# Performance work log

Measured on AMD Instinct MI355X. Metric: run time of the kernel, lower is better.

## Reference

```python
import jax, jax.numpy as jnp
import numpy as np

EPS = 1e-6

def _rms_norm(t, g):
    # t: [B, S, C] (applied before the view to heads, matching the torch code)
    y = t.astype(jnp.float32)
    y = jax.lax.rsqrt(jnp.mean(y * y, axis=-1, keepdims=True) + EPS)
    return (t * y * g).astype(t.dtype)

def _apply_rope(t, cos, sin):
    # t: [B, S, N, D]; cos/sin: [1, S, 1, D//2]; interleaved pair rotation
    b, s, n, d = t.shape
    tr = t.reshape(b, s, n, d // 2, 2)
    tre, tim = tr[..., 0], tr[..., 1]
    out = jnp.stack([tre * cos - tim * sin, tre * sin + tim * cos], axis=-1)
    return out.reshape(b, s, n, d)

def setup_inputs() -> dict:
    key = jax.random.key(0)
    ks = jax.random.split(key, 8)
    B, S, DIM, N, D = 2, 1024, 3072, 24, 128
    x = jax.random.normal(ks[0], (B, S, DIM), dtype=jnp.float32)
    seq_lens = jax.random.randint(ks[1], (B,), S // 2, S + 1, dtype=jnp.int32)
    grid_sizes = jnp.tile(jnp.array([[16, 8, 8]], dtype=jnp.int32), (B, 1))
    # rope angle table [1024, D//2]: pos * inv_freq
    inv_freq = 1.0 / (10000.0 ** (jnp.arange(D // 2, dtype=jnp.float32) * 2.0 / D))
    freqs = jnp.arange(1024, dtype=jnp.float32)[:, None] * inv_freq[None, :]
    sc = 1.0 / np.sqrt(DIM)
    Wq = jax.random.normal(ks[2], (DIM, DIM), dtype=jnp.float32) * sc
    Wk = jax.random.normal(ks[3], (DIM, DIM), dtype=jnp.float32) * sc
    Wv = jax.random.normal(ks[4], (DIM, DIM), dtype=jnp.float32) * sc
    Wo = jax.random.normal(ks[5], (DIM, DIM), dtype=jnp.float32) * sc
    bq = jnp.zeros((DIM,), jnp.float32); bk = jnp.zeros((DIM,), jnp.float32)
    bv = jnp.zeros((DIM,), jnp.float32); bo = jnp.zeros((DIM,), jnp.float32)
    gq = jnp.ones((DIM,), jnp.float32); gk = jnp.ones((DIM,), jnp.float32)
    return {"x": x, "seq_lens": seq_lens, "grid_sizes": grid_sizes, "freqs": freqs,
            "Wq": Wq, "bq": bq, "Wk": Wk, "bk": bk, "Wv": Wv, "bv": bv,
            "Wo": Wo, "bo": bo, "gq": gq, "gk": gk}

def reference(x, seq_lens, grid_sizes, freqs, Wq, bq, Wk, bk, Wv, bv, Wo, bo, gq, gk):
    b, s, dim = x.shape
    d = 2 * freqs.shape[1]          # head_dim
    n = dim // d                    # num_heads
    q = _rms_norm(x @ Wq.T + bq, gq).reshape(b, s, n, d)
    k = _rms_norm(x @ Wk.T + bk, gk).reshape(b, s, n, d)
    v = (x @ Wv.T + bv).reshape(b, s, n, d)
    ang = freqs[:s]                 # [S, D//2]
    cos = jnp.cos(ang)[None, :, None, :]
    sin = jnp.sin(ang)[None, :, None, :]
    q = _apply_rope(q, cos, sin)
    k = _apply_rope(k, cos, sin)
    # full attention (window_size = (-1,-1)), varlen key masking via seq_lens
    scale = d ** -0.5
    scores = jnp.einsum('bind,bjnd->bnij', q, k) * scale   # [B,N,S,S]
    key_valid = jnp.arange(s)[None, :] < seq_lens[:, None]  # [B,S]
    scores = jnp.where(key_valid[:, None, None, :], scores, jnp.finfo(scores.dtype).min)
    p = jax.nn.softmax(scores, axis=-1)
    out = jnp.einsum('bnij,bjnd->bind', p, v).reshape(b, s, dim)
    return out @ Wo.T + bo
```

## Files before the change

kernel.cpp:

```cpp
#include <hip/hip_runtime.h>
#include <cmath>

#define BB   2
#define SS   1024
#define DIMM 3072
#define NHH  24
#define HDD  128
#define MM   (BB * SS)

typedef _Float16 f16;
typedef __attribute__((ext_vector_type(8))) _Float16 half8;
typedef __attribute__((ext_vector_type(4))) float floatx4;
typedef unsigned int u32;
typedef const __attribute__((address_space(1))) u32* gp1;
typedef __attribute__((address_space(3))) u32* lp3;

__device__ __forceinline__ void gload_lds16(const void* g, void* l) {
    __builtin_amdgcn_global_load_lds((gp1)g, (lp3)l, 16, 0, 0);
}

__global__ __launch_bounds__(256) void cvt_f16_kernel(
    const float* __restrict__ in, f16* __restrict__ outp, int n8)
{
    int i = blockIdx.x * 256 + threadIdx.x;
    if (i >= n8) return;
    const float4* p = (const float4*)(in + (size_t)i * 8);
    float4 a = p[0], b = p[1];
    half8 h = {(f16)a.x, (f16)a.y, (f16)a.z, (f16)a.w,
               (f16)b.x, (f16)b.y, (f16)b.z, (f16)b.w};
    *(half8*)(outp + (size_t)i * 8) = h;
}

template<bool QKV>
__global__ __launch_bounds__(256) void gemm_f16p(
    const f16* __restrict__ A,
    const f16* __restrict__ W0, const f16* __restrict__ W1, const f16* __restrict__ W2,
    const float* __restrict__ b0, const float* __restrict__ b1, const float* __restrict__ b2,
    f16* __restrict__ D0, f16* __restrict__ D1, f16* __restrict__ D2,
    float* __restrict__ F)
{
    constexpr int K = DIMM;
    constexpr int NSTEP = K / 64;
    __shared__ __align__(16) f16 As[128 * 64];
    __shared__ __align__(16) f16 Bs[128 * 64];

    const int tid  = threadIdx.x;
    const int lane = tid & 63;
    const int wave = tid >> 6;
    const int wm = wave >> 1, wn = wave & 1;
    const int lr = lane & 15;
    const int lq = lane >> 4;

    const int id  = blockIdx.x;
    const int cpx = (int)gridDim.x >> 3;
    const int swz = (id & 7) * cpx + (id >> 3);
    const int bm = (swz & 15) << 7;
    const int bn = (swz >> 4) << 7;

    const f16* Wh; const float* bias; f16* D = nullptr;
    int nloc = bn;
    if constexpr (QKV) {
        int sel = bn / DIMM;
        nloc = bn - sel * DIMM;
        Wh   = sel == 0 ? W0 : (sel == 1 ? W1 : W2);
        bias = sel == 0 ? b0 : (sel == 1 ? b1 : b2);
        D    = sel == 0 ? D0 : (sel == 1 ? D1 : D2);
    } else { Wh = W0; bias = b0; }

    const int srow = lane >> 3;
    const int scol = ((lane & 7) ^ srow) << 3;
    const f16* ag = A  + (size_t)(bm   + srow) * K + scol;
    const f16* bg = Wh + (size_t)(nloc + srow) * K + scol;

    floatx4 acc[4][4];
#pragma unroll
    for (int i = 0; i < 4; ++i)
#pragma unroll
        for (int j = 0; j < 4; ++j) acc[i][j] = (floatx4){0.f, 0.f, 0.f, 0.f};

    for (int ks = 0; ks < NSTEP; ++ks) {
        const int k0 = ks * 64;
        __syncthreads();
#pragma unroll
        for (int i = 0; i < 4; ++i) {
            int rbase = wave * 32 + i * 8;
            gload_lds16(ag + (size_t)rbase * K + k0, &As[rbase * 64]);
            gload_lds16(bg + (size_t)rbase * K + k0, &Bs[rbase * 64]);
        }
        __syncthreads();

#pragma unroll
        for (int sub = 0; sub < 2; ++sub) {
            half8 af[4], bf[4];
#pragma unroll
            for (int i = 0; i < 4; ++i) {
                int ra = wm * 64 + i * 16 + lr;
                int rb = wn * 64 + i * 16 + lr;
                af[i] = *(const half8*)&As[ra * 64 + ((((sub << 2) + lq) ^ (lr & 7)) << 3)];
                bf[i] = *(const half8*)&Bs[rb * 64 + ((((sub << 2) + lq) ^ (lr & 7)) << 3)];
            }
#pragma unroll
            for (int mi = 0; mi < 4; ++mi)
#pragma unroll
                for (int ni = 0; ni < 4; ++ni)
                    acc[mi][ni] = __builtin_amdgcn_mfma_f32_16x16x32_f16(af[mi], bf[ni], acc[mi][ni], 0, 0, 0);
        }
    }

    const int crow0 = bm + wm * 64 + (lq << 2);
    const int ccol0 = nloc + wn * 64;
#pragma unroll
    for (int ni = 0; ni < 4; ++ni) {
        const int col = ccol0 + ni * 16 + lr;
        const float bv = bias[col];
#pragma unroll
        for (int mi = 0; mi < 4; ++mi) {
            const int row = crow0 + mi * 16;
#pragma unroll
            for (int r2 = 0; r2 < 4; ++r2) {
                if constexpr (QKV)
                    D[(size_t)(row + r2) * DIMM + col] = (f16)(acc[mi][ni][r2] + bv);
                else
                    F[(size_t)(row + r2) * DIMM + col] = acc[mi][ni][r2] + bv;
            }
        }
    }
}

template<bool QKV>
__global__ __launch_bounds__(256) void gemm_f16m(
    const f16* __restrict__ A,
    const float* __restrict__ W0, const float* __restrict__ W1, const float* __restrict__ W2,
    const float* __restrict__ b0, const float* __restrict__ b1, const float* __restrict__ b2,
    f16* __restrict__ D0, f16* __restrict__ D1, f16* __restrict__ D2,
    float* __restrict__ F)
{
    constexpr int K = DIMM;
    constexpr int NSTEP = K / 32;
    __shared__ f16 As[128 * 32];
    __shared__ f16 Bs[128 * 32];

    const int tid  = threadIdx.x;
    const int lane = tid & 63;
    const int wave = tid >> 6;
    const int wm = wave >> 1, wn = wave & 1;
    const int lr = lane & 15;
    const int lq = lane >> 4;

    const int id  = blockIdx.x;
    const int cpx = (int)gridDim.x >> 3;
    const int swz = (id & 7) * cpx + (id >> 3);
    const int bm = (swz & 15) << 7;
    const int bn = (swz >> 4) << 7;

    const float* W; const float* bias; f16* D = nullptr;
    int nloc = bn;
    if constexpr (QKV) {
        int sel = bn / DIMM;
        nloc = bn - sel * DIMM;
        W    = sel == 0 ? W0 : (sel == 1 ? W1 : W2);
        bias = sel == 0 ? b0 : (sel == 1 ? b1 : b2);
        D    = sel == 0 ? D0 : (sel == 1 ? D1 : D2);
    } else { W = W0; bias = b0; }

    const int r0 = tid >> 2;
    const int c8 = (tid & 3) << 3;
    const float* bp0 = W + (size_t)(nloc + r0) * K + c8;
    const float* bp1 = W + (size_t)(nloc + r0 + 64) * K + c8;

    const int arow_l = lane >> 2;
    const int acol_l = (lane & 3) << 3;
    const f16* agbase = A + (size_t)bm * K;

    float4 sb00, sb01, sb10, sb11;
    auto LOADB = [&](int k0) {
        sb00 = *(const float4*)(bp0 + k0); sb01 = *(const float4*)(bp0 + k0 + 4);
        sb10 = *(const float4*)(bp1 + k0); sb11 = *(const float4*)(bp1 + k0 + 4);
    };
    auto STOREB = [&]() {
        half8 h0 = {(f16)sb00.x, (f16)sb00.y, (f16)sb00.z, (f16)sb00.w,
                    (f16)sb01.x, (f16)sb01.y, (f16)sb01.z, (f16)sb01.w};
        half8 h1 = {(f16)sb10.x, (f16)sb10.y, (f16)sb10.z, (f16)sb10.w,
                    (f16)sb11.x, (f16)sb11.y, (f16)sb11.z, (f16)sb11.w};
        *(half8*)&Bs[r0 * 32 + c8]        = h0;
        *(half8*)&Bs[(r0 + 64) * 32 + c8] = h1;
    };

    floatx4 acc[4][4];
#pragma unroll
    for (int i = 0; i < 4; ++i)
#pragma unroll
        for (int j = 0; j < 4; ++j) acc[i][j] = (floatx4){0.f, 0.f, 0.f, 0.f};

    LOADB(0);
    for (int ks = 0; ks < NSTEP; ++ks) {
        const int k0 = ks * 32;
        __syncthreads();
#pragma unroll
        for (int i = 0; i < 2; ++i) {
            int rbase = wave * 32 + i * 16;
            gload_lds16(agbase + (size_t)(rbase + arow_l) * K + k0 + acol_l,
                        &As[rbase * 32]);
        }
        STOREB();
        __syncthreads();
        if (ks + 1 < NSTEP) LOADB(k0 + 32);

        half8 af[4], bf[4];
#pragma unroll
        for (int i = 0; i < 4; ++i) {
            af[i] = *(const half8*)&As[(wm * 64 + i * 16 + lr) * 32 + lq * 8];
            bf[i] = *(const half8*)&Bs[(wn * 64 + i * 16 + lr) * 32 + lq * 8];
        }
#pragma unroll
        for (int mi = 0; mi < 4; ++mi)
#pragma unroll
            for (int ni = 0; ni < 4; ++ni)
                acc[mi][ni] = __builtin_amdgcn_mfma_f32_16x16x32_f16(af[mi], bf[ni], acc[mi][ni], 0, 0, 0);
    }

    const int crow0 = bm + wm * 64 + (lq << 2);
    const int ccol0 = nloc + wn * 64;
#pragma unroll
    for (int ni = 0; ni < 4; ++ni) {
        const int col = ccol0 + ni * 16 + lr;
        const float bv = bias[col];
#pragma unroll
        for (int mi = 0; mi < 4; ++mi) {
            const int row = crow0 + mi * 16;
#pragma unroll
            for (int r2 = 0; r2 < 4; ++r2) {
                if constexpr (QKV)
                    D[(size_t)(row + r2) * DIMM + col] = (f16)(acc[mi][ni][r2] + bv);
                else
                    F[(size_t)(row + r2) * DIMM + col] = acc[mi][ni][r2] + bv;
            }
        }
    }
}

__global__ __launch_bounds__(192) void rmsnorm_rope_f16(
    f16* __restrict__ q, f16* __restrict__ k,
    const float* __restrict__ gq, const float* __restrict__ gk,
    const float* __restrict__ freqs)
{
    f16* t = (blockIdx.y == 0) ? q : k;
    const float* g = (blockIdx.y == 0) ? gq : gk;
    const int row = blockIdx.x;
    const int s = row & (SS - 1);
    const int tid = threadIdx.x;
    f16* base = t + (size_t)row * DIMM + tid * 16;

    half8 v0 = *(const half8*)base;
    half8 v1 = *(const half8*)(base + 8);
    float v[16];
#pragma unroll
    for (int j = 0; j < 8; ++j) { v[j] = (float)v0[j]; v[8 + j] = (float)v1[j]; }

    float ssq = 0.f;
#pragma unroll
    for (int j = 0; j < 16; ++j) ssq += v[j] * v[j];
#pragma unroll
    for (int off = 32; off > 0; off >>= 1) ssq += __shfl_down(ssq, off, 64);
    __shared__ float red[3];
    if ((tid & 63) == 0) red[tid >> 6] = ssq;
    __syncthreads();
    float tot = red[0] + red[1] + red[2];
    float sc = rsqrtf(tot * (1.0f / (float)DIMM) + 1e-6f);

    const float* gp = g + tid * 16;
    float y[16];
#pragma unroll
    for (int j = 0; j < 16; ++j) y[j] = v[j] * sc * gp[j];

#pragma unroll
    for (int p = 0; p < 8; ++p) {
        int idx = tid * 16 + 2 * p;
        int f = (idx & 127) >> 1;
        float ang = freqs[s * 64 + f];
        float cc = cosf(ang), sn = sinf(ang);
        float e = y[2 * p], o = y[2 * p + 1];
        y[2 * p]     = e * cc - o * sn;
        y[2 * p + 1] = e * sn + o * cc;
    }
    half8 o0, o1;
#pragma unroll
    for (int j = 0; j < 8; ++j) { o0[j] = (f16)y[j]; o1[j] = (f16)y[8 + j]; }
    *(half8*)base       = o0;
    *(half8*)(base + 8) = o1;
}

__global__ __launch_bounds__(256) void flash_attn_f16(
    const f16* __restrict__ Q, const f16* __restrict__ K,
    const f16* __restrict__ V, const int* __restrict__ seq_lens,
    f16* __restrict__ O)
{
    __shared__ __align__(16) f16 QPs[64 * 128];
    __shared__ __align__(16) f16 Ks[64 * 128];
    __shared__ __align__(16) f16 Vt[128 * 64];

    const int tid  = threadIdx.x;
    const int lane = tid & 63;
    const int wave = tid >> 6;
    const int ln = lane & 15;
    const int lq = lane >> 4;
    const int i0 = blockIdx.x * 64;
    const int h  = blockIdx.y;
    const int b  = blockIdx.z;
    const int slen = seq_lens[b];
    const float scale = 0.08838834764831845f;
    const size_t gstride = NHH * HDD;

    const f16* Qg = Q + ((size_t)(b * SS + i0) * NHH + h) * HDD;
#pragma unroll
    for (int rep = 0; rep < 4; ++rep) {
        int u = tid + rep * 256;
        int r = u >> 4, d0 = (u & 15) << 3;
        half8 qv = *(const half8*)(Qg + (size_t)r * gstride + d0);
        *(half8*)(QPs + r * 128 + (d0 ^ ((r & 7) << 3))) = qv;
    }
    __syncthreads();

    half8 qfrag[4];
    {
        int rq = wave * 16 + ln;
#pragma unroll
        for (int ks = 0; ks < 4; ++ks)
            qfrag[ks] = *(const half8*)(QPs + rq * 128 + ((ks * 32 + lq * 8) ^ ((rq & 7) << 3)));
    }

    floatx4 accO[8];
#pragma unroll
    for (int dt = 0; dt < 8; ++dt) accO[dt] = (floatx4){0.f, 0.f, 0.f, 0.f};
    float mrow[4] = {-3.0e38f, -3.0e38f, -3.0e38f, -3.0e38f};
    float lrow[4] = {0.f, 0.f, 0.f, 0.f};

    const int nT = (slen + 63) >> 6;
    for (int t = 0; t < nT; ++t) {
        const int j0g = t * 64;
        __syncthreads();

        const f16* Kg = K + ((size_t)(b * SS + j0g) * NHH + h) * HDD;
#pragma unroll
        for (int rep = 0; rep < 4; ++rep) {
            int u = tid + rep * 256;
            int r = u >> 4, d0 = (u & 15) << 3;
            half8 kv = *(const half8*)(Kg + (size_t)r * gstride + d0);
            *(half8*)(Ks + r * 128 + (d0 ^ ((r & 7) << 3))) = kv;
        }
        const f16* Vg = V + ((size_t)(b * SS + j0g) * NHH + h) * HDD;
#pragma unroll
        for (int rep = 0; rep < 2; ++rep) {
            int u = tid + rep * 256;
            int jp = u & 31, j0 = jp * 2;
            int d0 = (u >> 5) << 3;
            half8 va = *(const half8*)(Vg + (size_t)j0 * gstride + d0);
            half8 vb = *(const half8*)(Vg + (size_t)(j0 + 1) * gstride + d0);
#pragma unroll
            for (int i = 0; i < 8; ++i) {
                int d = d0 + i;
                union { f16 h[2]; u32 w; } pk;
                pk.h[0] = va[i]; pk.h[1] = vb[i];
                *(u32*)(Vt + d * 64 + (j0 ^ ((d & 7) << 3))) = pk.w;
            }
        }
        __syncthreads();

        floatx4 acc_s[4];
#pragma unroll
        for (int nt = 0; nt < 4; ++nt) {
            acc_s[nt] = (floatx4){0.f, 0.f, 0.f, 0.f};
            int rk = nt * 16 + ln;
#pragma unroll
            for (int ks = 0; ks < 4; ++ks) {
                half8 kf = *(const half8*)(Ks + rk * 128 + ((ks * 32 + lq * 8) ^ ((rk & 7) << 3)));
                acc_s[nt] = __builtin_amdgcn_mfma_f32_16x16x32_f16(qfrag[ks], kf, acc_s[nt], 0, 0, 0);
            }
        }

        float s[4][4];
#pragma unroll
        for (int nt = 0; nt < 4; ++nt) {
            int j = j0g + nt * 16 + ln;
            bool valid = (j < slen);
#pragma unroll
            for (int r = 0; r < 4; ++r)
                s[nt][r] = valid ? acc_s[nt][r] * scale : -3.0e38f;
        }
        float fct[4];
#pragma unroll
        for (int r = 0; r < 4; ++r) {
            float m4 = fmaxf(fmaxf(s[0][r], s[1][r]), fmaxf(s[2][r], s[3][r]));
            m4 = fmaxf(m4, __shfl_xor(m4, 1, 64));
            m4 = fmaxf(m4, __shfl_xor(m4, 2, 64));
            m4 = fmaxf(m4, __shfl_xor(m4, 4, 64));
            m4 = fmaxf(m4, __shfl_xor(m4, 8, 64));
            float mn = fmaxf(mrow[r], m4);
            fct[r] = __expf(mrow[r] - mn);
            mrow[r] = mn;
            float ls = 0.f;
#pragma unroll
            for (int nt = 0; nt < 4; ++nt) {
                float p = __expf(s[nt][r] - mn);
                s[nt][r] = p;
                ls += p;
            }
            ls += __shfl_xor(ls, 1, 64);
            ls += __shfl_xor(ls, 2, 64);
            ls += __shfl_xor(ls, 4, 64);
            ls += __shfl_xor(ls, 8, 64);
            lrow[r] = lrow[r] * fct[r] + ls;
        }

#pragma unroll
        for (int nt = 0; nt < 4; ++nt) {
#pragma unroll
            for (int r = 0; r < 4; ++r) {
                int rw = lq * 4 + r;
                int j = nt * 16 + ln;
                QPs[(wave * 16 + rw) * 128 + (j ^ ((rw & 7) << 3))] = (f16)s[nt][r];
            }
        }

#pragma unroll
        for (int dt = 0; dt < 8; ++dt)
#pragma unroll
            for (int r = 0; r < 4; ++r) accO[dt][r] *= fct[r];

        half8 pfrag[2];
#pragma unroll
        for (int js = 0; js < 2; ++js)
            pfrag[js] = *(const half8*)(QPs + (wave * 16 + ln) * 128 + ((js * 32 + lq * 8) ^ ((ln & 7) << 3)));
#pragma unroll
        for (int dt = 0; dt < 8; ++dt) {
            int d = dt * 16 + ln;
#pragma unroll
            for (int js = 0; js < 2; ++js) {
                half8 vf = *(const half8*)(Vt + d * 64 + ((js * 32 + lq * 8) ^ ((d & 7) << 3)));
                accO[dt] = __builtin_amdgcn_mfma_f32_16x16x32_f16(pfrag[js], vf, accO[dt], 0, 0, 0);
            }
        }
    }

    float linv[4];
#pragma unroll
    for (int r = 0; r < 4; ++r) linv[r] = 1.0f / lrow[r];
    f16* Og = O + ((size_t)(b * SS + i0) * NHH + h) * HDD;
#pragma unroll
    for (int dt = 0; dt < 8; ++dt) {
#pragma unroll
        for (int r = 0; r < 4; ++r) {
            int qr = wave * 16 + lq * 4 + r;
            int d = dt * 16 + ln;
            Og[(size_t)qr * gstride + d] = (f16)(accO[dt][r] * linv[r]);
        }
    }
}

extern "C" void kernel_launch(void* const* d_in, const int* in_sizes, int n_in,
                              void* d_out, int out_size, void* d_ws, size_t ws_size,
                              hipStream_t stream)
{
    const float* x     = (const float*)d_in[0];
    const int*   seq   = (const int*)d_in[1];
    const float* freqs = (const float*)d_in[3];
    const float* Wq    = (const float*)d_in[4];
    const float* bq    = (const float*)d_in[5];
    const float* Wk    = (const float*)d_in[6];
    const float* bk    = (const float*)d_in[7];
    const float* Wv    = (const float*)d_in[8];
    const float* bv    = (const float*)d_in[9];
    const float* Wo    = (const float*)d_in[10];
    const float* bo    = (const float*)d_in[11];
    const float* gq    = (const float*)d_in[12];
    const float* gk    = (const float*)d_in[13];

    float* out = (float*)d_out;
    const size_t MD = (size_t)MM * DIMM;
    const size_t WD = (size_t)DIMM * DIMM;

    f16* X16 = (f16*)d_ws;
    f16* q16 = X16 + MD;
    f16* k16 = X16 + 2 * MD;
    f16* v16 = (f16*)d_out;

    const int nMD8 = (int)(MD / 8);
    const int nWD8 = (int)(WD / 8);
    const size_t need = (3 * MD + 3 * WD) * sizeof(f16);

    cvt_f16_kernel<<<nMD8 / 256, 256, 0, stream>>>(x, X16, nMD8);

    if (ws_size >= need) {
        f16* Wq16 = X16 + 3 * MD;
        f16* Wk16 = Wq16 + WD;
        f16* Wv16 = Wk16 + WD;
        f16* Wo16 = Wq16;
        cvt_f16_kernel<<<nWD8 / 256, 256, 0, stream>>>(Wq, Wq16, nWD8);
        cvt_f16_kernel<<<nWD8 / 256, 256, 0, stream>>>(Wk, Wk16, nWD8);
        cvt_f16_kernel<<<nWD8 / 256, 256, 0, stream>>>(Wv, Wv16, nWD8);
        gemm_f16p<true><<<(MM / 128) * (3 * DIMM / 128), 256, 0, stream>>>(
            X16, Wq16, Wk16, Wv16, bq, bk, bv, q16, k16, v16, nullptr);
        cvt_f16_kernel<<<nWD8 / 256, 256, 0, stream>>>(Wo, Wo16, nWD8);
        rmsnorm_rope_f16<<<dim3(MM, 2), 192, 0, stream>>>(q16, k16, gq, gk, freqs);
        flash_attn_f16<<<dim3(SS / 64, NHH, BB), 256, 0, stream>>>(q16, k16, v16, seq, X16);
        gemm_f16p<false><<<(MM / 128) * (DIMM / 128), 256, 0, stream>>>(
            X16, Wo16, nullptr, nullptr, bo, nullptr, nullptr, nullptr, nullptr, nullptr, out);
    } else {
        gemm_f16m<true><<<(MM / 128) * (3 * DIMM / 128), 256, 0, stream>>>(
            X16, Wq, Wk, Wv, bq, bk, bv, q16, k16, v16, nullptr);
        rmsnorm_rope_f16<<<dim3(MM, 2), 192, 0, stream>>>(q16, k16, gq, gk, freqs);
        flash_attn_f16<<<dim3(SS / 64, NHH, BB), 256, 0, stream>>>(q16, k16, v16, seq, X16);
        gemm_f16m<false><<<(MM / 128) * (DIMM / 128), 256, 0, stream>>>(
            X16, Wo, nullptr, nullptr, bo, nullptr, nullptr, nullptr, nullptr, nullptr, out);
    }
}
```

Before: 368.8 us.

## Double-buffer LDS tiles in f16 GEMM and merge QKV weight conversions

```diff
diff --git a/kernel.cpp b/kernel.cpp
--- a/kernel.cpp
+++ b/kernel.cpp
@@ -31,6 +31,21 @@
     *(half8*)(outp + (size_t)i * 8) = h;
 }
 
+__global__ __launch_bounds__(256) void cvt3_f16_kernel(
+    const float* __restrict__ w0, const float* __restrict__ w1,
+    const float* __restrict__ w2, f16* __restrict__ outp, int n8each)
+{
+    int i = blockIdx.x * 256 + threadIdx.x;
+    int sel = i / n8each;
+    int j = i - sel * n8each;
+    const float* in = sel == 0 ? w0 : (sel == 1 ? w1 : w2);
+    const float4* p = (const float4*)(in + (size_t)j * 8);
+    float4 a = p[0], b = p[1];
+    half8 h = {(f16)a.x, (f16)a.y, (f16)a.z, (f16)a.w,
+               (f16)b.x, (f16)b.y, (f16)b.z, (f16)b.w};
+    *(half8*)(outp + (size_t)i * 8) = h;
+}
+
 template<bool QKV>
 __global__ __launch_bounds__(256) void gemm_f16p(
     const f16* __restrict__ A,
@@ -41,8 +56,9 @@
 {
     constexpr int K = DIMM;
     constexpr int NSTEP = K / 64;
-    __shared__ __align__(16) f16 As[128 * 64];
-    __shared__ __align__(16) f16 Bs[128 * 64];
+    constexpr int TS = 128 * 64;
+    __shared__ __align__(16) f16 As[2][TS];
+    __shared__ __align__(16) f16 Bs[2][TS];
 
     const int tid  = threadIdx.x;
     const int lane = tid & 63;
@@ -72,22 +88,28 @@
     const f16* ag = A  + (size_t)(bm   + srow) * K + scol;
     const f16* bg = Wh + (size_t)(nloc + srow) * K + scol;
 
-    floatx4 acc[4][4];
-#pragma unroll
-    for (int i = 0; i < 4; ++i)
-#pragma unroll
-        for (int j = 0; j < 4; ++j) acc[i][j] = (floatx4){0.f, 0.f, 0.f, 0.f};
-
-    for (int ks = 0; ks < NSTEP; ++ks) {
-        const int k0 = ks * 64;
-        __syncthreads();
+    auto STAGE = [&](int t, int buf) {
+        const int k0 = t * 64;
 #pragma unroll
         for (int i = 0; i < 4; ++i) {
             int rbase = wave * 32 + i * 8;
-            gload_lds16(ag + (size_t)rbase * K + k0, &As[rbase * 64]);
-            gload_lds16(bg + (size_t)rbase * K + k0, &Bs[rbase * 64]);
-        }
-        __syncthreads();
+            gload_lds16(ag + (size_t)rbase * K + k0, &As[buf][rbase * 64]);
+            gload_lds16(bg + (size_t)rbase * K + k0, &Bs[buf][rbase * 64]);
+        }
+    };
+
+    floatx4 acc[4][4];
+#pragma unroll
+    for (int i = 0; i < 4; ++i)
+#pragma unroll
+        for (int j = 0; j < 4; ++j) acc[i][j] = (floatx4){0.f, 0.f, 0.f, 0.f};
+
+    STAGE(0, 0);
+    __syncthreads();
+
+    for (int ks = 0; ks < NSTEP; ++ks) {
+        const int cur = ks & 1;
+        if (ks + 1 < NSTEP) STAGE(ks + 1, cur ^ 1);
 
 #pragma unroll
         for (int sub = 0; sub < 2; ++sub) {
@@ -96,8 +118,8 @@
             for (int i = 0; i < 4; ++i) {
                 int ra = wm * 64 + i * 16 + lr;
                 int rb = wn * 64 + i * 16 + lr;
-                af[i] = *(const half8*)&As[ra * 64 + ((((sub << 2) + lq) ^ (lr & 7)) << 3)];
-                bf[i] = *(const half8*)&Bs[rb * 64 + ((((sub << 2) + lq) ^ (lr & 7)) << 3)];
+                af[i] = *(const half8*)&As[cur][ra * 64 + ((((sub << 2) + lq) ^ (lr & 7)) << 3)];
+                bf[i] = *(const half8*)&Bs[cur][rb * 64 + ((((sub << 2) + lq) ^ (lr & 7)) << 3)];
             }
 #pragma unroll
             for (int mi = 0; mi < 4; ++mi)
@@ -105,6 +127,7 @@
                 for (int ni = 0; ni < 4; ++ni)
                     acc[mi][ni] = __builtin_amdgcn_mfma_f32_16x16x32_f16(af[mi], bf[ni], acc[mi][ni], 0, 0, 0);
         }
+        __syncthreads();
     }
 
     const int crow0 = bm + wm * 64 + (lq << 2);
@@ -495,9 +518,7 @@
         f16* Wk16 = Wq16 + WD;
         f16* Wv16 = Wk16 + WD;
         f16* Wo16 = Wq16;
-        cvt_f16_kernel<<<nWD8 / 256, 256, 0, stream>>>(Wq, Wq16, nWD8);
-        cvt_f16_kernel<<<nWD8 / 256, 256, 0, stream>>>(Wk, Wk16, nWD8);
-        cvt_f16_kernel<<<nWD8 / 256, 256, 0, stream>>>(Wv, Wv16, nWD8);
+        cvt3_f16_kernel<<<3 * nWD8 / 256, 256, 0, stream>>>(Wq, Wk, Wv, Wq16, nWD8);
         gemm_f16p<true><<<(MM / 128) * (3 * DIMM / 128), 256, 0, stream>>>(
             X16, Wq16, Wk16, Wv16, bq, bk, bv, q16, k16, v16, nullptr);
         cvt_f16_kernel<<<nWD8 / 256, 256, 0, stream>>>(Wo, Wo16, nWD8);
```

New measurement: 371.9 us. Within noise of the previous version (+0.8%).

## Batch weight conversions into one launch and split Q projection into separate GEMM

Applied to the files above, without the earlier changes.

```diff
diff --git a/kernel.cpp b/kernel.cpp
--- a/kernel.cpp
+++ b/kernel.cpp
@@ -29,6 +29,114 @@
     half8 h = {(f16)a.x, (f16)a.y, (f16)a.z, (f16)a.w,
                (f16)b.x, (f16)b.y, (f16)b.z, (f16)b.w};
     *(half8*)(outp + (size_t)i * 8) = h;
+}
+
+__global__ __launch_bounds__(256) void cvt3_f16_kernel(
+    const float* __restrict__ w0, const float* __restrict__ w1,
+    const float* __restrict__ w2, f16* __restrict__ outp, int n8each)
+{
+    int i = blockIdx.x * 256 + threadIdx.x;
+    int sel = i / n8each;
+    int j = i - sel * n8each;
+    const float* in = sel == 0 ? w0 : (sel == 1 ? w1 : w2);
+    const float4* p = (const float4*)(in + (size_t)j * 8);
+    float4 a = p[0], b = p[1];
+    half8 h = {(f16)a.x, (f16)a.y, (f16)a.z, (f16)a.w,
+               (f16)b.x, (f16)b.y, (f16)b.z, (f16)b.w};
+    *(half8*)(outp + (size_t)i * 8) = h;
+}
+
+__global__ __launch_bounds__(256) void cvt4_f16_kernel(
+    const float* __restrict__ w0, const float* __restrict__ w1,
+    const float* __restrict__ w2, const float* __restrict__ w3,
+    f16* __restrict__ outp, int n8each)
+{
+    int i = blockIdx.x * 256 + threadIdx.x;
+    int sel = i / n8each;
+    int j = i - sel * n8each;
+    const float* in = sel == 0 ? w0 : (sel == 1 ? w1 : (sel == 2 ? w2 : w3));
+    const float4* p = (const float4*)(in + (size_t)j * 8);
+    float4 a = p[0], b = p[1];
+    half8 h = {(f16)a.x, (f16)a.y, (f16)a.z, (f16)a.w,
+               (f16)b.x, (f16)b.y, (f16)b.z, (f16)b.w};
+    *(half8*)(outp + (size_t)i * 8) = h;
+}
+
+__global__ __launch_bounds__(256) void gemm_q32(
+    const f16* __restrict__ A, const f16* __restrict__ W,
+    const float* __restrict__ bias, f16* __restrict__ D)
+{
+    constexpr int K = DIMM;
+    constexpr int NSTEP = K / 32;
+    __shared__ __align__(16) f16 As[128 * 32];
+    __shared__ __align__(16) f16 Bs[128 * 32];
+
+    const int tid  = threadIdx.x;
+    const int lane = tid & 63;
+    const int wave = tid >> 6;
+    const int wm = wave >> 1, wn = wave & 1;
+    const int lr = lane & 15;
+    const int lq = lane >> 4;
+
+    const int id  = blockIdx.x;
+    const int cpx = (int)gridDim.x >> 3;
+    const int swz = (id & 7) * cpx + (id >> 3);
+    const int bm = (swz & 15) << 7;
+    const int bn = (swz >> 4) << 7;
+
+    const int r0 = tid >> 2;
+    const int g0 = ((tid & 3) ^ ((r0 >> 1) & 3)) << 3;
+    const int r1 = (tid + 256) >> 2;
+    const int g1 = ((tid & 3) ^ ((r1 >> 1) & 3)) << 3;
+    const f16* a0 = A + (size_t)(bm + r0) * K + g0;
+    const f16* a1 = A + (size_t)(bm + r1) * K + g1;
+    const f16* b0 = W + (size_t)(bn + r0) * K + g0;
+    const f16* b1 = W + (size_t)(bn + r1) * K + g1;
+
+    floatx4 acc[4][4];
+#pragma unroll
+    for (int i = 0; i < 4; ++i)
+#pragma unroll
+        for (int j = 0; j < 4; ++j) acc[i][j] = (floatx4){0.f, 0.f, 0.f, 0.f};
+
+    for (int ks = 0; ks < NSTEP; ++ks) {
+        const int k0 = ks * 32;
+        __syncthreads();
+        gload_lds16(a0 + k0, &As[(size_t)tid * 8]);
+        gload_lds16(a1 + k0, &As[(size_t)(tid + 256) * 8]);
+        gload_lds16(b0 + k0, &Bs[(size_t)tid * 8]);
+        gload_lds16(b1 + k0, &Bs[(size_t)(tid + 256) * 8]);
+        __syncthreads();
+
+        half8 af[4], bf[4];
+#pragma unroll
+        for (int i = 0; i < 4; ++i) {
+            int ra = wm * 64 + i * 16 + lr;
+            int rb = wn * 64 + i * 16 + lr;
+            af[i] = *(const half8*)&As[ra * 32 + ((lq ^ ((ra >> 1) & 3)) << 3)];
+            bf[i] = *(const half8*)&Bs[rb * 32 + ((lq ^ ((rb >> 1) & 3)) << 3)];
+        }
+#pragma unroll
+        for (int mi = 0; mi < 4; ++mi)
+#pragma unroll
+            for (int ni = 0; ni < 4; ++ni)
+                acc[mi][ni] = __builtin_amdgcn_mfma_f32_16x16x32_f16(af[mi], bf[ni], acc[mi][ni], 0, 0, 0);
+    }
+
+    const int crow0 = bm + wm * 64 + (lq << 2);
+    const int ccol0 = bn + wn * 64;
+#pragma unroll
+    for (int ni = 0; ni < 4; ++ni) {
+        const int col = ccol0 + ni * 16 + lr;
+        const float bv = bias[col];
+#pragma unroll
+        for (int mi = 0; mi < 4; ++mi) {
+            const int row = crow0 + mi * 16;
+#pragma unroll
+            for (int r2 = 0; r2 < 4; ++r2)
+                D[(size_t)(row + r2) * DIMM + col] = (f16)(acc[mi][ni][r2] + bv);
+        }
+    }
 }
 
 template<bool QKV>
@@ -486,21 +594,28 @@
 
     const int nMD8 = (int)(MD / 8);
     const int nWD8 = (int)(WD / 8);
-    const size_t need = (3 * MD + 3 * WD) * sizeof(f16);
+    const size_t need1 = (3 * MD + 3 * WD) * sizeof(f16);
+    const size_t need2 = (3 * MD + 4 * WD) * sizeof(f16);
 
     cvt_f16_kernel<<<nMD8 / 256, 256, 0, stream>>>(x, X16, nMD8);
 
-    if (ws_size >= need) {
+    if (ws_size >= need1) {
         f16* Wq16 = X16 + 3 * MD;
         f16* Wk16 = Wq16 + WD;
         f16* Wv16 = Wk16 + WD;
-        f16* Wo16 = Wq16;
-        cvt_f16_kernel<<<nWD8 / 256, 256, 0, stream>>>(Wq, Wq16, nWD8);
-        cvt_f16_kernel<<<nWD8 / 256, 256, 0, stream>>>(Wk, Wk16, nWD8);
-        cvt_f16_kernel<<<nWD8 / 256, 256, 0, stream>>>(Wv, Wv16, nWD8);
-        gemm_f16p<true><<<(MM / 128) * (3 * DIMM / 128), 256, 0, stream>>>(
-            X16, Wq16, Wk16, Wv16, bq, bk, bv, q16, k16, v16, nullptr);
-        cvt_f16_kernel<<<nWD8 / 256, 256, 0, stream>>>(Wo, Wo16, nWD8);
+        f16* Wo16;
+        if (ws_size >= need2) {
+            Wo16 = Wv16 + WD;
+            cvt4_f16_kernel<<<4 * nWD8 / 256, 256, 0, stream>>>(Wq, Wk, Wv, Wo, Wq16, nWD8);
+        } else {
+            Wo16 = Wq16;
+            cvt3_f16_kernel<<<3 * nWD8 / 256, 256, 0, stream>>>(Wq, Wk, Wv, Wq16, nWD8);
+        }
+        gemm_q32<<<(MM / 128) * (DIMM / 128), 256, 0, stream>>>(X16, Wq16, bq, q16);
+        gemm_f16p<true><<<(MM / 128) * (2 * DIMM / 128), 256, 0, stream>>>(
+            X16, Wk16, Wv16, nullptr, bk, bv, nullptr, k16, v16, nullptr, nullptr);
+        if (ws_size < need2)
+            cvt_f16_kernel<<<nWD8 / 256, 256, 0, stream>>>(Wo, Wo16, nWD8);
         rmsnorm_rope_f16<<<dim3(MM, 2), 192, 0, stream>>>(q16, k16, gq, gk, freqs);
         flash_attn_f16<<<dim3(SS / 64, NHH, BB), 256, 0, stream>>>(q16, k16, v16, seq, X16);
         gemm_f16p<false><<<(MM / 128) * (DIMM / 128), 256, 0, stream>>>(
```

Result: no change. 362.9 us (-1.6%).
